# Kernel tuning notes

Hardware: AMD Instinct MI355X
Metric: run time of the kernel (lower is better)

Reference implementation:

```python
import jax, jax.numpy as jnp
import numpy as np

B, N, F, T, E, OUT = 16, 5000, 8, 12, 160000, 64


def setup_inputs() -> dict:
    key = jax.random.key(0)
    ks = jax.random.split(key, 20)
    d = {}
    d["x"] = jax.random.normal(ks[0], (B, N, F, T), dtype=jnp.float32)
    d["edge_index"] = jax.random.randint(ks[1], (2, E), 0, N, dtype=jnp.int32)
    def p(k, shape, scale=0.1):
        return jax.random.normal(k, shape, dtype=jnp.float32) * scale
    i = 2
    for g in ("z", "r", "h"):
        d[f"W{g}"] = p(ks[i], (F, OUT)); i += 1        # GCNConv weight
        d[f"b{g}"] = p(ks[i], (OUT,)); i += 1           # GCNConv bias
        d[f"L{g}"] = p(ks[i], (2 * OUT, OUT)); i += 1   # gate Linear weight
        d[f"lb{g}"] = p(ks[i], (OUT,)); i += 1          # gate Linear bias
    d["att"] = p(ks[i], (T,)); i += 1                   # A3TGCN attention logits
    d["fcW"] = p(ks[i], (OUT, T)); i += 1               # final Linear 64->periods
    d["fcb"] = p(ks[i], (T,))
    return d


def _gcn(xs, W, b, src, dst, norm, n_nodes):
    # xs: [M, N, F] -> D^{-1/2}(A+I)D^{-1/2} (xs W) + b
    support = xs @ W                                    # [M, N, OUT]
    msg = support[:, src, :] * norm[None, :, None]      # gather at source
    agg = jax.vmap(lambda m: jax.ops.segment_sum(m, dst, num_segments=n_nodes))(msg)
    return agg + b


def reference(x, edge_index, Wz, bz, Lz, lbz, Wr, br, Lr, lbr, Wh, bh, Lh, lbh, att, fcW, fcb):
    b_sz, n_nodes, _, periods = x.shape
    src, dst = edge_index[0], edge_index[1]
    loop = jnp.arange(n_nodes, dtype=src.dtype)
    src = jnp.concatenate([src, loop])                  # add self loops
    dst = jnp.concatenate([dst, loop])
    deg = jax.ops.segment_sum(jnp.ones(src.shape, jnp.float32), dst, num_segments=n_nodes)
    dinv = jnp.where(deg > 0, jax.lax.rsqrt(deg), 0.0)
    norm = dinv[src] * dinv[dst]                        # symmetric GCN normalization

    # In A3TGCN the hidden state is never carried across periods (stays zero),
    # so all periods are independent: fold T into the batch axis.
    xs = jnp.moveaxis(x, 3, 0).reshape(periods * b_sz, n_nodes, x.shape[2])
    H = jnp.zeros((periods * b_sz, n_nodes, Wz.shape[1]), x.dtype)

    Z = jax.nn.sigmoid(jnp.concatenate([_gcn(xs, Wz, bz, src, dst, norm, n_nodes), H], -1) @ Lz + lbz)
    R = jax.nn.sigmoid(jnp.concatenate([_gcn(xs, Wr, br, src, dst, norm, n_nodes), H], -1) @ Lr + lbr)
    Ht = jnp.tanh(jnp.concatenate([_gcn(xs, Wh, bh, src, dst, norm, n_nodes), H * R], -1) @ Lh + lbh)
    Hnew = Z * H + (1.0 - Z) * Ht                       # [T*B, N, 64]

    Hs = Hnew.reshape(periods, b_sz, n_nodes, -1)
    Hacc = jnp.einsum('t,tbnh->bnh', jax.nn.softmax(att), Hs)
    return Hacc @ fcW + fcb                             # [B, N, periods]
```

## Files before the change

### kernel.cpp

```cpp
#include <hip/hip_runtime.h>

#define NN 5000
#define FF 8
#define TT 12
#define EE 160000
#define HH 64
#define EN (EE + NN)
#define CAP (EN + 7 * NN + 64)
#define XBSTRIDE 1920000
#define BSOFF    15360000

typedef float f2  __attribute__((ext_vector_type(2)));
typedef float f4v __attribute__((ext_vector_type(4)));

#define LOG2E 1.44269504088896340736f


__global__ void k_count(const int* __restrict__ dst, int* __restrict__ deg) {
    int i = blockIdx.x * blockDim.x + threadIdx.x;
    if (i < EE) atomicAdd(&deg[dst[i]], 1);
}

__global__ __launch_bounds__(1024) void k_scan_prep(
    const int* __restrict__ deg, int* __restrict__ offs, int* __restrict__ cursor,
    float* __restrict__ dinv,
    const float* __restrict__ Wz, const float* __restrict__ bz,
    const float* __restrict__ Lz, const float* __restrict__ lbz,
    const float* __restrict__ Wh, const float* __restrict__ bh,
    const float* __restrict__ Lh, const float* __restrict__ lbh,
    const float* __restrict__ att, const float* __restrict__ fcW,
    float* __restrict__ G, float* __restrict__ C, float* __restrict__ sm,
    float* __restrict__ fcwT) {
    int tid = threadIdx.x;
    if (blockIdx.x == 0) {
        __shared__ int s[1024];
        int base = tid * 5;
        int pad[5], real[5];
        int part = 0;
#pragma unroll
        for (int j = 0; j < 5; ++j) {
            int n = base + j;
            int c = (n < NN) ? deg[n] + 1 : 0;
            real[j] = c;
            pad[j] = (c + 7) & ~7;
            part += pad[j];
        }
        s[tid] = part;
        __syncthreads();
        for (int d = 1; d < 1024; d <<= 1) {
            int v = (tid >= d) ? s[tid - d] : 0;
            __syncthreads();
            s[tid] += v;
            __syncthreads();
        }
        int run = s[tid] - part;
#pragma unroll
        for (int j = 0; j < 5; ++j) {
            int n = base + j;
            if (n < NN) {
                offs[n] = run;
                cursor[n] = run;
                dinv[n] = rsqrtf((float)real[j]);
                run += pad[j];
            }
        }
        if (tid == 1023) offs[NN] = s[1023];
    } else {
        if (tid < 1024) {
            int g = tid >> 9, rem = tid & 511, f = rem >> 6, o = rem & 63;
            const float* W = g ? Wh : Wz;
            const float* L = g ? Lh : Lz;
            float acc = 0.f;
            for (int k = 0; k < 64; ++k) acc += W[f * 64 + k] * L[k * 64 + o];
            G[tid] = acc * (g ? 2.0f * LOG2E : LOG2E);
        }
        if (tid < 128) {
            int g = tid >> 6, o = tid & 63;
            const float* b = g ? bh : bz;
            const float* L = g ? Lh : Lz;
            const float* lb = g ? lbh : lbz;
            float acc = lb[o];
            for (int k = 0; k < 64; ++k) acc += b[k] * L[k * 64 + o];
            C[tid] = acc * (g ? 2.0f * LOG2E : LOG2E);
        }
        if (tid < 768) {
            int t = tid >> 6, o = tid & 63;
            fcwT[tid] = fcW[o * TT + t];
        }
        if (tid == 0) {
            float m = att[0];
            for (int t = 1; t < TT; ++t) m = fmaxf(m, att[t]);
            float e[TT], ss = 0.f;
            for (int t = 0; t < TT; ++t) { e[t] = __expf(att[t] - m); ss += e[t]; }
            for (int t = 0; t < TT; ++t) sm[t] = e[t] / ss;
        }
    }
}

__global__ void k_fill(const int* __restrict__ src, const int* __restrict__ dst,
                       int* cursor, const float* __restrict__ dinv,
                       int2* __restrict__ cedge) {
    int i = blockIdx.x * blockDim.x + threadIdx.x;
    if (i < EE) {
        int s = src[i], d = dst[i];
        int p = atomicAdd(&cursor[d], 1);
        cedge[p] = make_int2(s, __float_as_int(dinv[s] * dinv[d]));
    } else if (i < EN) {
        int n = i - EE;
        int p = atomicAdd(&cursor[n], 1);
        cedge[p] = make_int2(n, __float_as_int(dinv[n] * dinv[n]));
    }
}


#define E2S(Q)                                                    \
    {                                                             \
        unsigned a0_ = (unsigned)(Q).x * 384u + voff;             \
        unsigned a1_ = (unsigned)(Q).z * 384u + voff;             \
        f4v v0_ = *(const f4v*)(xbb + a0_);                       \
        f4v v1_ = *(const f4v*)(xbb + a1_);                       \
        accA += __int_as_float((Q).y) * v0_;                      \
        accB += __int_as_float((Q).w) * v1_;                      \
    }

__global__ __launch_bounds__(256) void k_node(
    const float* __restrict__ x, const int* __restrict__ offs,
    const int2* __restrict__ cedge,
    const float* __restrict__ G, const float* __restrict__ C,
    const float* __restrict__ sm, const float* __restrict__ fcwT,
    const float* __restrict__ fcb, float* __restrict__ out) {
    __shared__ __align__(16) float xals[4][2][96];
    __shared__ __align__(16) float hl[4][2][64];

    const int wid = threadIdx.x >> 6;
    const int lane = threadIdx.x & 63;
    const int bp = blockIdx.x & 7;
    const int n = (blockIdx.x >> 3) * 4 + wid;

    int r0 = __builtin_amdgcn_readfirstlane(offs[n]);
    int r1 = __builtin_amdgcn_readfirstlane(offs[n + 1]);

    const char* xbb = (const char*)x + (size_t)bp * XBSTRIDE;

    if (lane < 48) {
        const unsigned voff = (unsigned)(lane / 24) * BSOFF + (unsigned)(lane % 24) * 16u;
        f4v accA = {0.f, 0.f, 0.f, 0.f};
        f4v accB = {0.f, 0.f, 0.f, 0.f};

        const int4* ce = (const int4*)cedge;
        int c = r0 >> 1;
        const int c1 = r1 >> 1;
        int4 A0 = ce[c], A1 = ce[c + 1], A2 = ce[c + 2], A3 = ce[c + 3];
        int4 B0 = ce[c + 4], B1 = ce[c + 5], B2 = ce[c + 6], B3 = ce[c + 7];
        while (true) {
            int4 D0 = A0, D1 = A1, D2 = A2, D3 = A3;
            A0 = B0; A1 = B1; A2 = B2; A3 = B3;
            B0 = ce[c + 8]; B1 = ce[c + 9]; B2 = ce[c + 10]; B3 = ce[c + 11];
            E2S(D0) E2S(D1) E2S(D2) E2S(D3)
            c += 4;
            if (c >= c1) break;
        }
        f4v acc = accA + accB;
        *(f4v*)&xals[wid][lane / 24][(lane % 24) * 4] = acc;
    }

    float gz[FF], gh[FF];
#pragma unroll
    for (int f = 0; f < FF; ++f) {
        gz[f] = G[f * 64 + lane];
        gh[f] = G[512 + f * 64 + lane];
    }
    float cz = C[lane], ch = C[64 + lane];
    float smv[TT];
#pragma unroll
    for (int t = 0; t < TT; ++t) smv[t] = sm[t];

#pragma unroll
    for (int bs = 0; bs < 2; ++bs) {
        float hacc0 = 0.f, hacc1 = 0.f;
#pragma unroll
        for (int tq = 0; tq < 3; ++tq) {
            f4v xq[FF];
#pragma unroll
            for (int f = 0; f < FF; ++f)
                xq[f] = *(const f4v*)&xals[wid][bs][f * TT + tq * 4];
#pragma unroll
            for (int half = 0; half < 2; ++half) {
                f2 az = {cz, cz}, ah = {ch, ch};
#pragma unroll
                for (int f = 0; f < FF; ++f) {
                    f2 v = half ? xq[f].hi : xq[f].lo;
                    az += v * gz[f];
                    ah += v * gh[f];
                }
                {
                    float ea = exp2f(az[0]);
                    float e2h = exp2f(ah[0]);
                    float num = e2h - 1.0f;
                    float den = (1.0f + ea) * (1.0f + e2h);
                    hacc0 += smv[tq * 4 + half * 2] * num * __builtin_amdgcn_rcpf(den);
                }
                {
                    float ea = exp2f(az[1]);
                    float e2h = exp2f(ah[1]);
                    float num = e2h - 1.0f;
                    float den = (1.0f + ea) * (1.0f + e2h);
                    hacc1 += smv[tq * 4 + half * 2 + 1] * num * __builtin_amdgcn_rcpf(den);
                }
            }
        }
        hl[wid][bs][lane] = hacc0 + hacc1;
    }

    if (lane < 24) {
        int bs = lane / 12, t = lane % 12;
        float acc = fcb[t];
#pragma unroll
        for (int o4 = 0; o4 < 16; ++o4) {
            f4v h4 = *(const f4v*)&hl[wid][bs][o4 * 4];
            f4v w4 = *(const f4v*)&fcwT[t * 64 + o4 * 4];
            acc += h4[0] * w4[0] + h4[1] * w4[1] + h4[2] * w4[2] + h4[3] * w4[3];
        }
        int b = bp + bs * 8;
        out[((size_t)b * NN + n) * TT + t] = acc;
    }
}

extern "C" void kernel_launch(void* const* d_in, const int* in_sizes, int n_in,
                              void* d_out, int out_size, void* d_ws, size_t ws_size,
                              hipStream_t stream) {
    const float* x   = (const float*)d_in[0];
    const int*   ei  = (const int*)d_in[1];
    const float* Wz  = (const float*)d_in[2];
    const float* bz  = (const float*)d_in[3];
    const float* Lz  = (const float*)d_in[4];
    const float* lbz = (const float*)d_in[5];
    const float* Wh  = (const float*)d_in[10];
    const float* bh  = (const float*)d_in[11];
    const float* Lh  = (const float*)d_in[12];
    const float* lbh = (const float*)d_in[13];
    const float* att = (const float*)d_in[14];
    const float* fcW = (const float*)d_in[15];
    const float* fcb = (const float*)d_in[16];
    float* out = (float*)d_out;

    const int* src = ei;
    const int* dst = ei + EE;

    int2*  cedge  = (int2*)d_ws;
    int*   deg    = (int*)(cedge + CAP);
    int*   cursor = deg + NN;
    int*   offs   = cursor + NN;
    float* dinv   = (float*)(offs + NN + 1);
    float* G      = dinv + NN;
    float* C      = G + 1024;
    float* sm     = C + 128;
    float* fcwT   = sm + 16;

    (void)hipMemsetAsync(d_ws, 0, (size_t)CAP * 8 + (size_t)NN * 4, stream);
    hipLaunchKernelGGL(k_count, dim3((EE + 255) / 256), dim3(256), 0, stream, dst, deg);
    hipLaunchKernelGGL(k_scan_prep, dim3(2), dim3(1024), 0, stream,
                       deg, offs, cursor, dinv,
                       Wz, bz, Lz, lbz, Wh, bh, Lh, lbh, att, fcW, G, C, sm, fcwT);
    hipLaunchKernelGGL(k_fill, dim3((EN + 255) / 256), dim3(256), 0, stream,
                       src, dst, cursor, dinv, cedge);
    hipLaunchKernelGGL(k_node, dim3(1250 * 8), dim3(256), 0, stream,
                       x, offs, cedge, G, C, sm, fcwT, fcb, out);
}
```

Before: 139.5 us.

## Use persistent XCC-aware work-stealing blocks and zero only edge padding

Replaces the one-block-per-(node group, batch pair) grid with 2048 persistent blocks that pull node groups from per-batch-pair atomic queues. Each block starts on the queue chosen by its XCC id so that blocks on the same die share the same x slice in L2. Constant weights are staged once per block into LDS. The full workspace memset is replaced by zeroing only the padding slots of the CSR edge array inside the scan kernel. This costs extra atomics and block-wide barriers per work item.

```diff
diff --git a/kernel.cpp b/kernel.cpp
--- a/kernel.cpp
+++ b/kernel.cpp
@@ -9,6 +9,7 @@
 #define CAP (EN + 7 * NN + 64)
 #define XBSTRIDE 1920000
 #define BSOFF    15360000
+#define NGRP     1250
 
 typedef float f2  __attribute__((ext_vector_type(2)));
 typedef float f4v __attribute__((ext_vector_type(4)));
@@ -23,7 +24,7 @@
 
 __global__ __launch_bounds__(1024) void k_scan_prep(
     const int* __restrict__ deg, int* __restrict__ offs, int* __restrict__ cursor,
-    float* __restrict__ dinv,
+    float* __restrict__ dinv, int2* __restrict__ cedge,
     const float* __restrict__ Wz, const float* __restrict__ bz,
     const float* __restrict__ Lz, const float* __restrict__ lbz,
     const float* __restrict__ Wh, const float* __restrict__ bh,
@@ -61,10 +62,16 @@
                 offs[n] = run;
                 cursor[n] = run;
                 dinv[n] = rsqrtf((float)real[j]);
+                for (int e = real[j]; e < pad[j]; ++e)
+                    cedge[run + e] = make_int2(0, 0);
                 run += pad[j];
             }
         }
-        if (tid == 1023) offs[NN] = s[1023];
+        if (tid == 1023) {
+            offs[NN] = s[1023];
+            for (int k = 0; k < 64; ++k)
+                cedge[s[1023] + k] = make_int2(0, 0);
+        }
     } else {
         if (tid < 1024) {
             int g = tid >> 9, rem = tid & 511, f = rem >> 6, o = rem & 63;
@@ -113,14 +120,14 @@
 }
 
 
-#define E2S(Q)                                                    \
+#define E2C(Q)                                                    \
     {                                                             \
         unsigned a0_ = (unsigned)(Q).x * 384u + voff;             \
         unsigned a1_ = (unsigned)(Q).z * 384u + voff;             \
         f4v v0_ = *(const f4v*)(xbb + a0_);                       \
         f4v v1_ = *(const f4v*)(xbb + a1_);                       \
-        accA += __int_as_float((Q).y) * v0_;                      \
-        accB += __int_as_float((Q).w) * v1_;                      \
+        acc0 += __int_as_float((Q).y) * v0_;                      \
+        acc1 += __int_as_float((Q).w) * v1_;                      \
     }
 
 __global__ __launch_bounds__(256) void k_node(
@@ -128,101 +135,139 @@
     const int2* __restrict__ cedge,
     const float* __restrict__ G, const float* __restrict__ C,
     const float* __restrict__ sm, const float* __restrict__ fcwT,
-    const float* __restrict__ fcb, float* __restrict__ out) {
+    const float* __restrict__ fcb, int* __restrict__ qctr,
+    float* __restrict__ out) {
+    __shared__ __align__(16) float Glds[1024];
+    __shared__ __align__(16) float Clds[128];
+    __shared__ __align__(16) float fcw[768];
+    __shared__ __align__(16) float sml[16];
     __shared__ __align__(16) float xals[4][2][96];
     __shared__ __align__(16) float hl[4][2][64];
-
-    const int wid = threadIdx.x >> 6;
-    const int lane = threadIdx.x & 63;
-    const int bp = blockIdx.x & 7;
-    const int n = (blockIdx.x >> 3) * 4 + wid;
-
-    int r0 = __builtin_amdgcn_readfirstlane(offs[n]);
-    int r1 = __builtin_amdgcn_readfirstlane(offs[n + 1]);
-
-    const char* xbb = (const char*)x + (size_t)bp * XBSTRIDE;
-
-    if (lane < 48) {
-        const unsigned voff = (unsigned)(lane / 24) * BSOFF + (unsigned)(lane % 24) * 16u;
-        f4v accA = {0.f, 0.f, 0.f, 0.f};
-        f4v accB = {0.f, 0.f, 0.f, 0.f};
-
-        const int4* ce = (const int4*)cedge;
-        int c = r0 >> 1;
-        const int c1 = r1 >> 1;
-        int4 A0 = ce[c], A1 = ce[c + 1], A2 = ce[c + 2], A3 = ce[c + 3];
-        int4 B0 = ce[c + 4], B1 = ce[c + 5], B2 = ce[c + 6], B3 = ce[c + 7];
-        while (true) {
-            int4 D0 = A0, D1 = A1, D2 = A2, D3 = A3;
-            A0 = B0; A1 = B1; A2 = B2; A3 = B3;
-            B0 = ce[c + 8]; B1 = ce[c + 9]; B2 = ce[c + 10]; B3 = ce[c + 11];
-            E2S(D0) E2S(D1) E2S(D2) E2S(D3)
-            c += 4;
-            if (c >= c1) break;
-        }
-        f4v acc = accA + accB;
-        *(f4v*)&xals[wid][lane / 24][(lane % 24) * 4] = acc;
-    }
+    __shared__ int gsh;
+
+    const int tid = threadIdx.x;
+    const int wid = tid >> 6;
+    const int lane = tid & 63;
+
+    ((f4v*)Glds)[tid] = ((const f4v*)G)[tid];
+    if (tid < 192) ((f4v*)fcw)[tid] = ((const f4v*)fcwT)[tid];
+    if (tid < 32) ((f4v*)Clds)[tid] = ((const f4v*)C)[tid];
+    if (tid < 12) sml[tid] = sm[tid];
+    __syncthreads();
 
     float gz[FF], gh[FF];
 #pragma unroll
     for (int f = 0; f < FF; ++f) {
-        gz[f] = G[f * 64 + lane];
-        gh[f] = G[512 + f * 64 + lane];
-    }
-    float cz = C[lane], ch = C[64 + lane];
+        gz[f] = Glds[f * 64 + lane];
+        gh[f] = Glds[512 + f * 64 + lane];
+    }
+    const float cz = Clds[lane], ch = Clds[64 + lane];
     float smv[TT];
 #pragma unroll
-    for (int t = 0; t < TT; ++t) smv[t] = sm[t];
-
-#pragma unroll
-    for (int bs = 0; bs < 2; ++bs) {
-        float hacc0 = 0.f, hacc1 = 0.f;
-#pragma unroll
-        for (int tq = 0; tq < 3; ++tq) {
-            f4v xq[FF];
-#pragma unroll
-            for (int f = 0; f < FF; ++f)
-                xq[f] = *(const f4v*)&xals[wid][bs][f * TT + tq * 4];
-#pragma unroll
-            for (int half = 0; half < 2; ++half) {
-                f2 az = {cz, cz}, ah = {ch, ch};
-#pragma unroll
-                for (int f = 0; f < FF; ++f) {
-                    f2 v = half ? xq[f].hi : xq[f].lo;
-                    az += v * gz[f];
-                    ah += v * gh[f];
+    for (int t = 0; t < TT; ++t) smv[t] = sml[t];
+
+    int myx;
+    asm volatile("s_getreg_b32 %0, hwreg(HW_REG_XCC_ID)" : "=s"(myx));
+    myx &= 7;
+
+    for (int p = 0; p < 8; ++p) {
+        const int bp = (myx + p) & 7;
+        const char* xbb = (const char*)x + (size_t)bp * XBSTRIDE;
+        for (;;) {
+            if (tid == 0) gsh = atomicAdd(&qctr[bp], 1);
+            __syncthreads();
+            const int grp = gsh;
+            __syncthreads();
+            if (grp >= NGRP) break;
+
+            const int n = grp * 4 + wid;
+            int r0 = __builtin_amdgcn_readfirstlane(offs[n]);
+            int r1 = __builtin_amdgcn_readfirstlane(offs[n + 1]);
+
+            if (lane < 48) {
+                const unsigned voff =
+                    (unsigned)(lane / 24) * BSOFF + (unsigned)(lane % 24) * 16u;
+                f4v acc0 = {0.f, 0.f, 0.f, 0.f};
+                f4v acc1 = {0.f, 0.f, 0.f, 0.f};
+                const int4* ce = (const int4*)cedge;
+                int c = r0 >> 1;
+                const int c1 = r1 >> 1;
+                int4 A0 = ce[c], A1 = ce[c + 1], A2 = ce[c + 2], A3 = ce[c + 3];
+                int4 B0 = ce[c + 4], B1 = ce[c + 5], B2 = ce[c + 6], B3 = ce[c + 7];
+                while (true) {
+                    int4 D0 = A0, D1 = A1, D2 = A2, D3 = A3;
+                    A0 = B0; A1 = B1; A2 = B2; A3 = B3;
+                    B0 = ce[c + 8]; B1 = ce[c + 9];
+                    B2 = ce[c + 10]; B3 = ce[c + 11];
+                    E2C(D0) E2C(D1) E2C(D2) E2C(D3)
+                    c += 4;
+                    if (c >= c1) break;
                 }
-                {
-                    float ea = exp2f(az[0]);
-                    float e2h = exp2f(ah[0]);
-                    float num = e2h - 1.0f;
-                    float den = (1.0f + ea) * (1.0f + e2h);
-                    hacc0 += smv[tq * 4 + half * 2] * num * __builtin_amdgcn_rcpf(den);
+                f4v acc = acc0 + acc1;
+                *(f4v*)&xals[wid][lane / 24][(lane % 24) * 4] = acc;
+            }
+
+#pragma unroll
+            for (int bs = 0; bs < 2; ++bs) {
+                float hacc0 = 0.f, hacc1 = 0.f;
+#pragma unroll
+                for (int tq = 0; tq < 3; ++tq) {
+                    f4v xq[FF];
+#pragma unroll
+                    for (int f = 0; f < FF; ++f)
+                        xq[f] = *(const f4v*)&xals[wid][bs][f * TT + tq * 4];
+#pragma unroll
+                    for (int half = 0; half < 2; ++half) {
+                        f2 az = {cz, cz}, ah = {ch, ch};
+#pragma unroll
+                        for (int f = 0; f < FF; ++f) {
+                            f2 v = half ? xq[f].hi : xq[f].lo;
+                            az += v * gz[f];
+                            ah += v * gh[f];
+                        }
+                        {
+                            float ea = exp2f(az[0]);
+                            float e2h = exp2f(ah[0]);
+                            float num = e2h - 1.0f;
+                            float den = (1.0f + ea) * (1.0f + e2h);
+                            hacc0 += smv[tq * 4 + half * 2] * num *
+                                     __builtin_amdgcn_rcpf(den);
+                        }
+                        {
+                            float ea = exp2f(az[1]);
+                            float e2h = exp2f(ah[1]);
+                            float num = e2h - 1.0f;
+                            float den = (1.0f + ea) * (1.0f + e2h);
+                            hacc1 += smv[tq * 4 + half * 2 + 1] * num *
+                                     __builtin_amdgcn_rcpf(den);
+                        }
+                    }
                 }
-                {
-                    float ea = exp2f(az[1]);
-                    float e2h = exp2f(ah[1]);
-                    float num = e2h - 1.0f;
-                    float den = (1.0f + ea) * (1.0f + e2h);
-                    hacc1 += smv[tq * 4 + half * 2 + 1] * num * __builtin_amdgcn_rcpf(den);
+                hl[wid][bs][lane] = hacc0 + hacc1;
+            }
+            __syncthreads();
+
+            if (tid < 96) {
+                int nw = tid / 24;
+                int rem = tid % 24;
+                int bs = rem / 12;
+                int t = rem % 12;
+                float acc = fcb[t];
+                const float* hrow = &hl[nw][bs][0];
+                const float* wrow = &fcw[t * 64];
+#pragma unroll
+                for (int o4 = 0; o4 < 16; ++o4) {
+                    f4v h4 = *(const f4v*)&hrow[o4 * 4];
+                    f4v w4 = *(const f4v*)&wrow[o4 * 4];
+                    acc += h4[0] * w4[0] + h4[1] * w4[1] +
+                           h4[2] * w4[2] + h4[3] * w4[3];
                 }
+                int b = bp + bs * 8;
+                int n2 = grp * 4 + nw;
+                out[((size_t)b * NN + n2) * TT + t] = acc;
             }
-        }
-        hl[wid][bs][lane] = hacc0 + hacc1;
-    }
-
-    if (lane < 24) {
-        int bs = lane / 12, t = lane % 12;
-        float acc = fcb[t];
-#pragma unroll
-        for (int o4 = 0; o4 < 16; ++o4) {
-            f4v h4 = *(const f4v*)&hl[wid][bs][o4 * 4];
-            f4v w4 = *(const f4v*)&fcwT[t * 64 + o4 * 4];
-            acc += h4[0] * w4[0] + h4[1] * w4[1] + h4[2] * w4[2] + h4[3] * w4[3];
-        }
-        int b = bp + bs * 8;
-        out[((size_t)b * NN + n) * TT + t] = acc;
+            __syncthreads();
+        }
     }
 }
 
@@ -248,7 +293,8 @@
     const int* dst = ei + EE;
 
     int2*  cedge  = (int2*)d_ws;
-    int*   deg    = (int*)(cedge + CAP);
+    int*   qctr   = (int*)(cedge + CAP);
+    int*   deg    = qctr + 16;
     int*   cursor = deg + NN;
     int*   offs   = cursor + NN;
     float* dinv   = (float*)(offs + NN + 1);
@@ -257,13 +303,13 @@
     float* sm     = C + 128;
     float* fcwT   = sm + 16;
 
-    (void)hipMemsetAsync(d_ws, 0, (size_t)CAP * 8 + (size_t)NN * 4, stream);
+    (void)hipMemsetAsync(qctr, 0, (16 + NN) * sizeof(int), stream);
     hipLaunchKernelGGL(k_count, dim3((EE + 255) / 256), dim3(256), 0, stream, dst, deg);
     hipLaunchKernelGGL(k_scan_prep, dim3(2), dim3(1024), 0, stream,
-                       deg, offs, cursor, dinv,
+                       deg, offs, cursor, dinv, cedge,
                        Wz, bz, Lz, lbz, Wh, bh, Lh, lbh, att, fcW, G, C, sm, fcwT);
     hipLaunchKernelGGL(k_fill, dim3((EN + 255) / 256), dim3(256), 0, stream,
                        src, dst, cursor, dinv, cedge);
-    hipLaunchKernelGGL(k_node, dim3(1250 * 8), dim3(256), 0, stream,
-                       x, offs, cedge, G, C, sm, fcwT, fcb, out);
-}
+    hipLaunchKernelGGL(k_node, dim3(2048), dim3(256), 0, stream,
+                       x, offs, cedge, G, C, sm, fcwT, fcb, qctr, out);
+}
```

After: 357.3 us. 156% more time.
